# Performance work log

Hardware: AMD Instinct MI355X
Metric: run time of the kernel (lower is better)

Reference implementation:

```python
import jax, jax.numpy as jnp
import numpy as np

D_MODEL, N_HEADS, D_FF = 1024, 16, 4096
NUM_FAMILIES, DICT_SIZE = 64, 16384
B, T = 2, 2048
EPS = 1e-6


def setup_inputs() -> dict:
    key = jax.random.key(0)
    ks = jax.random.split(key, 16)
    s = 0.02
    return {
        "x": jax.random.normal(ks[0], (B, T, D_MODEL), jnp.float32),
        "top_k": 8,
        "proto": jax.random.normal(ks[1], (NUM_FAMILIES, D_MODEL), jnp.float32) * s,
        "family_gate_w": jax.random.normal(ks[2], (NUM_FAMILIES, D_MODEL), jnp.float32) * s,
        "dict_w": jax.random.normal(ks[3], (DICT_SIZE, D_MODEL), jnp.float32) * s,
        "enc_w": jax.random.normal(ks[4], (DICT_SIZE, D_MODEL), jnp.float32) * s,
        "wq": jax.random.normal(ks[5], (D_MODEL, D_MODEL), jnp.float32) * s,
        "wk": jax.random.normal(ks[6], (D_MODEL, D_MODEL), jnp.float32) * s,
        "wv": jax.random.normal(ks[7], (D_MODEL, D_MODEL), jnp.float32) * s,
        "wo": jax.random.normal(ks[8], (D_MODEL, D_MODEL), jnp.float32) * s,
        "rel_templates": jax.random.normal(ks[9], (N_HEADS, D_MODEL // N_HEADS, D_MODEL // N_HEADS), jnp.float32) * s,
        "gate_proj_w": jax.random.normal(ks[10], (D_FF, D_MODEL), jnp.float32) * s,
        "up_proj_w": jax.random.normal(ks[11], (D_FF, D_MODEL), jnp.float32) * s,
        "down_proj_w": jax.random.normal(ks[12], (D_MODEL, D_FF), jnp.float32) * s,
        "norm1_w": jnp.ones((D_MODEL,), jnp.float32),
        "norm2_w": jnp.ones((D_MODEL,), jnp.float32),
        "bias_corr": jnp.zeros((D_MODEL,), jnp.float32),
    }


def _hc_norm(x, w):
    rms = jnp.sqrt(jnp.mean(x * x, axis=-1, keepdims=True) + EPS)
    return w * x / rms, jnp.mean(rms)


def _block(x, top_k, proto, family_gate_w, dict_w, enc_w, wq, wk, wv, wo,
           rel_templates, gate_proj_w, up_proj_w, down_proj_w,
           norm1_w, norm2_w, bias_corr):
    b, t, d = x.shape
    h = rel_templates.shape[0]
    dh = d // h
    m = dict_w.shape[0]

    # FamilyBasisPool
    family_scores = jax.nn.softmax(x @ family_gate_w.T, axis=-1)   # [b,t,K]
    basis = jnp.einsum('btk,kd->btd', family_scores, proto)

    # SparseOffsetDict on residual
    resid = x - basis
    coeffs = resid @ enc_w.T                                        # [b,t,M]
    topk_vals, topk_idx = jax.lax.top_k(coeffs, top_k)              # [b,t,k]
    # sparse scatter + einsum == gather rows of dictionary and weight them
    offset = jnp.einsum('btk,btkd->btd', topk_vals, dict_w[topk_idx])
    sparsity = jnp.sum(jnp.abs(topk_vals)) / (b * t * m)

    x_rec = basis + offset + bias_corr
    normed, e1 = _hc_norm(x_rec, norm1_w)

    # RelationProtocolLayer (k modulated by per-head templates)
    q = (normed @ wq.T).reshape(b, t, h, dh).transpose(0, 2, 1, 3)  # [b,h,t,dh]
    k = (normed @ wk.T).reshape(b, t, h, dh).transpose(0, 2, 1, 3)
    v = (normed @ wv.T).reshape(b, t, h, dh).transpose(0, 2, 1, 3)
    k_mod = jnp.einsum('bhtd,hde->bhte', k, rel_templates)
    attn = jax.nn.softmax(jnp.einsum('bhqd,bhkd->bhqk', q, k_mod) / jnp.sqrt(jnp.float32(dh)), axis=-1)
    out = jnp.einsum('bhqk,bhkd->bhqd', attn, v)
    out = out.transpose(0, 2, 1, 3).reshape(b, t, d) @ wo.T
    x = x + out

    normed2, e2 = _hc_norm(x, norm2_w)

    # ContextGatedRouter (sigmoid gate * silu up)
    gate = jax.nn.sigmoid(normed2 @ gate_proj_w.T)
    up = jax.nn.silu(normed2 @ up_proj_w.T)
    routed = (gate * up) @ down_proj_w.T
    x = x + routed
    return x, attn, family_scores, sparsity, e1, e2


def reference(x, top_k, proto, family_gate_w, dict_w, enc_w, wq, wk, wv, wo,
              rel_templates, gate_proj_w, up_proj_w, down_proj_w,
              norm1_w, norm2_w, bias_corr):
    return _block(x, top_k, proto, family_gate_w, dict_w, enc_w, wq, wk, wv, wo,
                  rel_templates, gate_proj_w, up_proj_w, down_proj_w,
                  norm1_w, norm2_w, bias_corr)
```

## Files before the change

kernel.cpp:

```cpp
#include <hip/hip_runtime.h>
#include <float.h>
#include <math.h>

#define D 1024
#define NF 64
#define MDICT 16384
#define NH 16
#define DH 64
#define TT 2048
#define ROWS 4096
#define DFF 4096

#define OUT_X     0LL
#define OUT_ATTN  4194304LL
#define OUT_FS    138412032LL
#define OUT_SPARS 138674176LL
#define OUT_E1    138674177LL
#define OUT_E2    138674178LL

typedef __attribute__((ext_vector_type(8))) short short8;
typedef __attribute__((ext_vector_type(4))) float f32x4;

__device__ inline unsigned short f2bf(float f) {
    unsigned int u = __float_as_uint(f);
    u = u + 0x7FFFu + ((u >> 16) & 1u);
    return (unsigned short)(u >> 16);
}
__device__ inline float bf2f(unsigned int s) {
    return __uint_as_float(s << 16);
}

__device__ inline float blk_sum(float v) {
    __shared__ float sb[4];
    int lane = threadIdx.x & 63, w = threadIdx.x >> 6;
#pragma unroll
    for (int o = 32; o; o >>= 1) v += __shfl_down(v, o);
    if (lane == 0) sb[w] = v;
    __syncthreads();
    float s = sb[0] + sb[1] + sb[2] + sb[3];
    __syncthreads();
    return s;
}

__device__ inline float blk_max(float v) {
    __shared__ float sm[4];
    int lane = threadIdx.x & 63, w = threadIdx.x >> 6;
#pragma unroll
    for (int o = 32; o; o >>= 1) v = fmaxf(v, __shfl_down(v, o));
    if (lane == 0) sm[w] = v;
    __syncthreads();
    float s = fmaxf(fmaxf(sm[0], sm[1]), fmaxf(sm[2], sm[3]));
    __syncthreads();
    return s;
}

template<int BM, int BN, bool OBF, bool ACONV>
__global__ __launch_bounds__(256) void gemm_mfma(
    const void* __restrict__ Abv, const unsigned short* __restrict__ Bb,
    void* __restrict__ Cbv, const float* __restrict__ addCb,
    int K, int lda, int ldb, int ldc, float alpha, int batchH,
    long long aOut, long long aIn, long long bOut, long long bIn,
    long long cOut, long long cIn)
{
    int z = blockIdx.z;
    int zo = z / batchH, zi = z - zo * batchH;
    long long aoff = zo * aOut + zi * aIn;
    const unsigned short* B = Bb + zo * bOut + zi * bIn;
    long long cbase = zo * cOut + zi * cIn;
    const float* addC = addCb ? (addCb + cbase) : nullptr;

    __shared__ __align__(16) unsigned short As[BM * 32];
    __shared__ __align__(16) unsigned short Bs[BN * 32];

    int tid = threadIdx.x;
    int lane = tid & 63, wave = tid >> 6;
    int wr = wave >> 1, wc = wave & 1;
    long long r0 = (long long)blockIdx.y * BM;
    long long c0 = (long long)blockIdx.x * BN;

    constexpr int TI = BM / 32;
    constexpr int TJ = BN / 32;
    constexpr int RA = BM * 4 / 256;
    constexpr int RB = BN * 4 / 256;

    f32x4 acc[TI][TJ] = {};
    int lm = lane & 15;
    int kq = (lane >> 4) * 8;

    for (int k0 = 0; k0 < K; k0 += 32) {
        __syncthreads();
#pragma unroll
        for (int r = 0; r < RB; r++) {
            int q = r * 256 + tid;
            const unsigned short* gp = B + (c0 + (q >> 2)) * (long long)ldb + k0 + (q & 3) * 8;
            unsigned short* lp = Bs + (r * 256 + (tid & 192)) * 8;
            __builtin_amdgcn_global_load_lds(
                (const __attribute__((address_space(1))) void*)gp,
                (__attribute__((address_space(3))) void*)lp, 16, 0, 0);
        }
        if (ACONV) {
            const float* A = (const float*)Abv + aoff;
#pragma unroll
            for (int r = 0; r < RA; r++) {
                int q = r * 256 + tid;
                const float* gp = A + (r0 + (q >> 2)) * (long long)lda + k0 + (q & 3) * 8;
                float4 v0 = *(const float4*)gp;
                float4 v1 = *(const float4*)(gp + 4);
                short8 f;
                f[0] = (short)f2bf(v0.x); f[1] = (short)f2bf(v0.y);
                f[2] = (short)f2bf(v0.z); f[3] = (short)f2bf(v0.w);
                f[4] = (short)f2bf(v1.x); f[5] = (short)f2bf(v1.y);
                f[6] = (short)f2bf(v1.z); f[7] = (short)f2bf(v1.w);
                *(short8*)&As[q * 8] = f;
            }
        } else {
            const unsigned short* A = (const unsigned short*)Abv + aoff;
#pragma unroll
            for (int r = 0; r < RA; r++) {
                int q = r * 256 + tid;
                const unsigned short* gp = A + (r0 + (q >> 2)) * (long long)lda + k0 + (q & 3) * 8;
                unsigned short* lp = As + (r * 256 + (tid & 192)) * 8;
                __builtin_amdgcn_global_load_lds(
                    (const __attribute__((address_space(1))) void*)gp,
                    (__attribute__((address_space(3))) void*)lp, 16, 0, 0);
            }
        }
        __syncthreads();
        short8 af[TI], bfr[TJ];
#pragma unroll
        for (int i = 0; i < TI; i++)
            af[i] = *(const short8*)&As[(wr * (BM / 2) + i * 16 + lm) * 32 + kq];
#pragma unroll
        for (int j = 0; j < TJ; j++)
            bfr[j] = *(const short8*)&Bs[(wc * (BN / 2) + j * 16 + lm) * 32 + kq];
#pragma unroll
        for (int i = 0; i < TI; i++)
#pragma unroll
            for (int j = 0; j < TJ; j++)
                acc[i][j] = __builtin_amdgcn_mfma_f32_16x16x32_bf16(af[i], bfr[j], acc[i][j], 0, 0, 0);
    }

#pragma unroll
    for (int i = 0; i < TI; i++) {
#pragma unroll
        for (int r = 0; r < 4; r++) {
            long long row = r0 + wr * (BM / 2) + i * 16 + (lane >> 4) * 4 + r;
#pragma unroll
            for (int j = 0; j < TJ; j++) {
                long long col = c0 + wc * (BN / 2) + j * 16 + lm;
                long long idx = row * (long long)ldc + col;
                float v = alpha * acc[i][j][r];
                if (addC) v += addC[idx];
                if (OBF) ((unsigned short*)Cbv)[cbase + idx] = f2bf(v);
                else     ((float*)Cbv)[cbase + idx] = v;
            }
        }
    }
}

__global__ __launch_bounds__(256) void cvt_bf16_kernel(
    const float* __restrict__ in, unsigned short* __restrict__ out, long long n4)
{
    long long i = (long long)blockIdx.x * 256 + threadIdx.x;
    long long stride = (long long)gridDim.x * 256;
    for (; i < n4; i += stride) {
        float4 v = ((const float4*)in)[i];
        uint2 p;
        p.x = (unsigned)f2bf(v.x) | ((unsigned)f2bf(v.y) << 16);
        p.y = (unsigned)f2bf(v.z) | ((unsigned)f2bf(v.w) << 16);
        ((uint2*)out)[i] = p;
    }
}

__global__ __launch_bounds__(64) void family_kernel(
    const float* __restrict__ x, const float* __restrict__ fgw,
    float* __restrict__ fs_out)
{
    __shared__ float xs[D];
    int r = blockIdx.x, f = threadIdx.x;
    const float4* x4 = (const float4*)(x + (long long)r * D);
    float4* xs4 = (float4*)xs;
#pragma unroll
    for (int i = 0; i < 4; i++) xs4[f + 64 * i] = x4[f + 64 * i];
    __syncthreads();
    const float4* w4 = (const float4*)(fgw + (long long)f * D);
    float acc = 0.f;
#pragma unroll 8
    for (int d = 0; d < D / 4; d++) {
        float4 w = w4[d];
        float4 xv = xs4[d];
        acc += w.x * xv.x + w.y * xv.y + w.z * xv.z + w.w * xv.w;
    }
    float mx = acc;
#pragma unroll
    for (int o = 32; o; o >>= 1) mx = fmaxf(mx, __shfl_xor(mx, o));
    float e = __expf(acc - mx);
    float s = e;
#pragma unroll
    for (int o = 32; o; o >>= 1) s += __shfl_xor(s, o);
    fs_out[(long long)r * NF + f] = e / s;
}

__global__ __launch_bounds__(256) void basis_kernel(
    const float* __restrict__ x, const float* __restrict__ fs,
    const float* __restrict__ proto, float* __restrict__ basis,
    unsigned short* __restrict__ resid_bf)
{
    __shared__ float Ss[NF];
    int r = blockIdx.x, tid = threadIdx.x;
    if (tid < NF) Ss[tid] = fs[(long long)r * NF + tid];
    __syncthreads();
    float4 acc = {0.f, 0.f, 0.f, 0.f};
    const float4* p4 = (const float4*)proto;
#pragma unroll 8
    for (int k = 0; k < NF; k++) {
        float s = Ss[k];
        float4 p = p4[k * (D / 4) + tid];
        acc.x += s * p.x; acc.y += s * p.y; acc.z += s * p.z; acc.w += s * p.w;
    }
    long long base = (long long)r * (D / 4) + tid;
    float4 xv = ((const float4*)x)[base];
    ((float4*)basis)[base] = acc;
    uint2 rp;
    rp.x = (unsigned)f2bf(xv.x - acc.x) | ((unsigned)f2bf(xv.y - acc.y) << 16);
    rp.y = (unsigned)f2bf(xv.z - acc.z) | ((unsigned)f2bf(xv.w - acc.w) << 16);
    ((uint2*)resid_bf)[base] = rp;
}

__device__ inline void ins8(float v, int idx, float* vs, int* is) {
    if (v <= vs[7]) return;
    vs[7] = v; is[7] = idx;
#pragma unroll
    for (int j = 7; j > 0; j--) {
        if (vs[j] > vs[j - 1]) {
            float tv = vs[j]; vs[j] = vs[j - 1]; vs[j - 1] = tv;
            int ti = is[j]; is[j] = is[j - 1]; is[j - 1] = ti;
        }
    }
}

__global__ __launch_bounds__(256) void topk_kernel(
    const float* __restrict__ coeffs, float* __restrict__ tkv,
    int* __restrict__ tki, float* __restrict__ spars_acc)
{
    __shared__ float sv[2624];
    __shared__ int   si[2624];
    int r = blockIdx.x, tid = threadIdx.x;
    const float* row = coeffs + (long long)r * MDICT;
    float vs[8]; int is[8];
#pragma unroll
    for (int j = 0; j < 8; j++) { vs[j] = -FLT_MAX; is[j] = -1; }
    for (int s = 0; s < MDICT / 256; s++) {
        int col = s * 256 + tid;
        ins8(row[col], col, vs, is);
    }
#pragma unroll
    for (int j = 0; j < 8; j++) { sv[tid * 8 + j] = vs[j]; si[tid * 8 + j] = is[j]; }
    __syncthreads();
    if (tid < 64) {
#pragma unroll
        for (int j = 0; j < 8; j++) { vs[j] = -FLT_MAX; is[j] = -1; }
        for (int e = tid * 32; e < tid * 32 + 32; e++) ins8(sv[e], si[e], vs, is);
#pragma unroll
        for (int j = 0; j < 8; j++) { sv[2048 + tid * 8 + j] = vs[j]; si[2048 + tid * 8 + j] = is[j]; }
    }
    __syncthreads();
    if (tid < 8) {
#pragma unroll
        for (int j = 0; j < 8; j++) { vs[j] = -FLT_MAX; is[j] = -1; }
        for (int e = 2048 + tid * 64; e < 2048 + tid * 64 + 64; e++) ins8(sv[e], si[e], vs, is);
#pragma unroll
        for (int j = 0; j < 8; j++) { sv[2560 + tid * 8 + j] = vs[j]; si[2560 + tid * 8 + j] = is[j]; }
    }
    __syncthreads();
    if (tid == 0) {
#pragma unroll
        for (int j = 0; j < 8; j++) { vs[j] = -FLT_MAX; is[j] = -1; }
        for (int e = 2560; e < 2624; e++) ins8(sv[e], si[e], vs, is);
        float s = 0.f;
#pragma unroll
        for (int j = 0; j < 8; j++) {
            tkv[r * 8 + j] = vs[j];
            tki[r * 8 + j] = is[j];
            s += fabsf(vs[j]);
        }
        atomicAdd(spars_acc, s);
    }
}

__global__ __launch_bounds__(256) void xrec_norm_kernel(
    const float* __restrict__ basis, const float* __restrict__ dictw,
    const float* __restrict__ bias, const float* __restrict__ nw,
    const float* __restrict__ tkv, const int* __restrict__ tki,
    unsigned short* __restrict__ normed_bf, float* __restrict__ e_acc)
{
    int r = blockIdx.x, tid = threadIdx.x;
    float vals[8]; int idxs[8];
#pragma unroll
    for (int j = 0; j < 8; j++) { vals[j] = tkv[r * 8 + j]; idxs[j] = tki[r * 8 + j]; }
    long long base = (long long)r * (D / 4) + tid;
    float4 acc = ((const float4*)basis)[base];
    float4 bv = ((const float4*)bias)[tid];
    acc.x += bv.x; acc.y += bv.y; acc.z += bv.z; acc.w += bv.w;
#pragma unroll
    for (int j = 0; j < 8; j++) {
        float4 dv = ((const float4*)dictw)[(long long)idxs[j] * (D / 4) + tid];
        float v = vals[j];
        acc.x += v * dv.x; acc.y += v * dv.y; acc.z += v * dv.z; acc.w += v * dv.w;
    }
    float ss = acc.x * acc.x + acc.y * acc.y + acc.z * acc.z + acc.w * acc.w;
    float tot = blk_sum(ss);
    float rms = sqrtf(tot / (float)D + 1e-6f);
    if (tid == 0) atomicAdd(e_acc, rms);
    float inv = 1.f / rms;
    float4 wv = ((const float4*)nw)[tid];
    uint2 o;
    o.x = (unsigned)f2bf(acc.x * wv.x * inv) | ((unsigned)f2bf(acc.y * wv.y * inv) << 16);
    o.y = (unsigned)f2bf(acc.z * wv.z * inv) | ((unsigned)f2bf(acc.w * wv.w * inv) << 16);
    ((uint2*)normed_bf)[base] = o;
}

__global__ __launch_bounds__(256) void rmsnorm_kernel(
    const float* __restrict__ xin, const float* __restrict__ nw,
    unsigned short* __restrict__ xout_bf, float* __restrict__ e_acc)
{
    int r = blockIdx.x, tid = threadIdx.x;
    long long base = (long long)r * (D / 4) + tid;
    float4 v = ((const float4*)xin)[base];
    float ss = v.x * v.x + v.y * v.y + v.z * v.z + v.w * v.w;
    float tot = blk_sum(ss);
    float rms = sqrtf(tot / (float)D + 1e-6f);
    if (tid == 0) atomicAdd(e_acc, rms);
    float inv = 1.f / rms;
    float4 wv = ((const float4*)nw)[tid];
    uint2 o;
    o.x = (unsigned)f2bf(v.x * wv.x * inv) | ((unsigned)f2bf(v.y * wv.y * inv) << 16);
    o.y = (unsigned)f2bf(v.z * wv.z * inv) | ((unsigned)f2bf(v.w * wv.w * inv) << 16);
    ((uint2*)xout_bf)[base] = o;
}

__global__ __launch_bounds__(256) void kmod_kernel(
    const unsigned short* __restrict__ kb, const float* __restrict__ rel,
    unsigned short* __restrict__ kmod_bf)
{
    __shared__ float Rs[64 * 64];
    int z = blockIdx.y;
    int b = z >> 4, h = z & 15;
    int tid = threadIdx.x;
    const float4* r4 = (const float4*)(rel + (long long)h * 4096);
    float4* Rs4 = (float4*)Rs;
#pragma unroll
    for (int i = 0; i < 4; i++) Rs4[tid + 256 * i] = r4[tid + 256 * i];
    __syncthreads();
    int e = tid & 63, tl = tid >> 6;
    int t = blockIdx.x * 4 + tl;
    const unsigned short* krow = kb + ((long long)(b * TT + t)) * D + h * DH;
    float acc = 0.f;
#pragma unroll
    for (int d4 = 0; d4 < 16; d4++) {
        uint2 p = *(const uint2*)&krow[d4 * 4];
        acc += bf2f(p.x & 0xFFFFu) * Rs[(d4 * 4 + 0) * 64 + e];
        acc += bf2f(p.x >> 16)     * Rs[(d4 * 4 + 1) * 64 + e];
        acc += bf2f(p.y & 0xFFFFu) * Rs[(d4 * 4 + 2) * 64 + e];
        acc += bf2f(p.y >> 16)     * Rs[(d4 * 4 + 3) * 64 + e];
    }
    kmod_bf[(long long)z * (TT * DH) + t * 64 + e] = f2bf(acc);
}

__global__ __launch_bounds__(256) void vtrans_kernel(
    const unsigned short* __restrict__ vb, unsigned short* __restrict__ vT)
{
    __shared__ unsigned short tile[64][68];
    int z = blockIdx.y, b = z >> 4, h = z & 15;
    int t0 = blockIdx.x * 64;
    int tid = threadIdx.x;
    int tr = tid >> 4;
    int dc = (tid & 15) * 4;
#pragma unroll
    for (int r = 0; r < 4; r++) {
        int t = tr + r * 16;
        uint2 p = *(const uint2*)&vb[((long long)(b * TT + t0 + t)) * D + h * DH + dc];
        tile[t][dc] = (unsigned short)(p.x & 0xFFFFu);
        tile[t][dc + 1] = (unsigned short)(p.x >> 16);
        tile[t][dc + 2] = (unsigned short)(p.y & 0xFFFFu);
        tile[t][dc + 3] = (unsigned short)(p.y >> 16);
    }
    __syncthreads();
#pragma unroll
    for (int r = 0; r < 4; r++) {
        int d = tr + r * 16;
        int t = (tid & 15) * 4;
        uint2 p;
        p.x = (unsigned)tile[t][d] | ((unsigned)tile[t + 1][d] << 16);
        p.y = (unsigned)tile[t + 2][d] | ((unsigned)tile[t + 3][d] << 16);
        *(uint2*)&vT[(long long)z * 64 * TT + (long long)d * TT + t0 + t] = p;
    }
}

__global__ __launch_bounds__(256) void softmax_kernel(float* __restrict__ attn)
{
    long long row = blockIdx.x;
    float4* p4 = (float4*)(attn + row * TT);
    int tid = threadIdx.x;
    float4 v0 = p4[tid], v1 = p4[tid + 256];
    float mx = fmaxf(fmaxf(fmaxf(v0.x, v0.y), fmaxf(v0.z, v0.w)),
                     fmaxf(fmaxf(v1.x, v1.y), fmaxf(v1.z, v1.w)));
    mx = blk_max(mx);
    v0.x = __expf(v0.x - mx); v0.y = __expf(v0.y - mx);
    v0.z = __expf(v0.z - mx); v0.w = __expf(v0.w - mx);
    v1.x = __expf(v1.x - mx); v1.y = __expf(v1.y - mx);
    v1.z = __expf(v1.z - mx); v1.w = __expf(v1.w - mx);
    float s = v0.x + v0.y + v0.z + v0.w + v1.x + v1.y + v1.z + v1.w;
    s = blk_sum(s);
    float inv = 1.f / s;
    v0.x *= inv; v0.y *= inv; v0.z *= inv; v0.w *= inv;
    v1.x *= inv; v1.y *= inv; v1.z *= inv; v1.w *= inv;
    p4[tid] = v0; p4[tid + 256] = v1;
}

__global__ __launch_bounds__(256) void gateup_kernel(
    unsigned short* __restrict__ g, const unsigned short* __restrict__ u, long long n4)
{
    long long i = (long long)blockIdx.x * 256 + threadIdx.x;
    long long stride = (long long)gridDim.x * 256;
    for (; i < n4; i += stride) {
        uint2 gp = ((uint2*)g)[i];
        uint2 up = ((const uint2*)u)[i];
        float gv[4] = { bf2f(gp.x & 0xFFFFu), bf2f(gp.x >> 16), bf2f(gp.y & 0xFFFFu), bf2f(gp.y >> 16) };
        float uv[4] = { bf2f(up.x & 0xFFFFu), bf2f(up.x >> 16), bf2f(up.y & 0xFFFFu), bf2f(up.y >> 16) };
        unsigned short h[4];
#pragma unroll
        for (int j = 0; j < 4; j++) {
            float r = (1.f / (1.f + __expf(-gv[j]))) * uv[j] * (1.f / (1.f + __expf(-uv[j])));
            h[j] = f2bf(r);
        }
        uint2 o;
        o.x = (unsigned)h[0] | ((unsigned)h[1] << 16);
        o.y = (unsigned)h[2] | ((unsigned)h[3] << 16);
        ((uint2*)g)[i] = o;
    }
}

__global__ void finalize_kernel(const float* __restrict__ scal, float* __restrict__ out)
{
    out[OUT_SPARS] = scal[0] / (float)((double)ROWS * (double)MDICT);
    out[OUT_E1] = scal[1] / (float)ROWS;
    out[OUT_E2] = scal[2] / (float)ROWS;
}

extern "C" void kernel_launch(void* const* d_in, const int* in_sizes, int n_in,
                              void* d_out, int out_size, void* d_ws, size_t ws_size,
                              hipStream_t stream) {
    const float* x     = (const float*)d_in[0];
    const float* proto = (const float*)d_in[2];
    const float* fgw   = (const float*)d_in[3];
    const float* dictw = (const float*)d_in[4];
    const float* encw  = (const float*)d_in[5];
    const float* wq    = (const float*)d_in[6];
    const float* wk    = (const float*)d_in[7];
    const float* wv    = (const float*)d_in[8];
    const float* wo    = (const float*)d_in[9];
    const float* rel   = (const float*)d_in[10];
    const float* gatew = (const float*)d_in[11];
    const float* upw   = (const float*)d_in[12];
    const float* downw = (const float*)d_in[13];
    const float* n1w   = (const float*)d_in[14];
    const float* n2w   = (const float*)d_in[15];
    const float* bias  = (const float*)d_in[16];
    float* out = (float*)d_out;
    float* ws  = (float*)d_ws;

    float*          basisf  = ws + 0;
    unsigned short* kb_bf   = (unsigned short*)(ws + 4194304);
    unsigned short* resid_bf= (unsigned short*)(ws + 6291456);
    unsigned short* norm_bf = (unsigned short*)(ws + 8388608);
    unsigned short* qb_bf   = (unsigned short*)(ws + 10485760);
    unsigned short* vb_bf   = (unsigned short*)(ws + 12582912);
    unsigned short* kmod_bf = (unsigned short*)(ws + 14680064);
    unsigned short* vT_bf   = (unsigned short*)(ws + 16777216);
    unsigned short* encw_bf = (unsigned short*)(ws + 18874368);
    unsigned short* up_bf   = (unsigned short*)(ws + 27262976);
    unsigned short* wq_bf   = (unsigned short*)(ws + 35651584);
    unsigned short* wk_bf   = (unsigned short*)(ws + 36175872);
    unsigned short* wv_bf   = (unsigned short*)(ws + 36700160);
    unsigned short* wo_bf   = (unsigned short*)(ws + 37224448);
    unsigned short* gatew_bf= (unsigned short*)(ws + 37748736);
    unsigned short* upw_bf  = (unsigned short*)(ws + 39845888);
    unsigned short* downw_bf= (unsigned short*)(ws + 41943040);
    float*          tkv     = ws + 44040192;
    int*            tki     = (int*)(ws + 44072960);
    float*          scal    = ws + 44105728;
    unsigned short* ctx_bf  = resid_bf;
    unsigned short* gate_bf = encw_bf;
    float*          xmid    = basisf;

    float* fs   = out + OUT_FS;
    float* attn = out + OUT_ATTN;
    float* coeffs = attn;

    hipMemsetAsync(scal, 0, 3 * sizeof(float), stream);

    cvt_bf16_kernel<<<2048, 256, 0, stream>>>(encw, encw_bf, (long long)MDICT * D / 4);
    cvt_bf16_kernel<<<256, 256, 0, stream>>>(wq, wq_bf, (long long)D * D / 4);
    cvt_bf16_kernel<<<256, 256, 0, stream>>>(wk, wk_bf, (long long)D * D / 4);
    cvt_bf16_kernel<<<256, 256, 0, stream>>>(wv, wv_bf, (long long)D * D / 4);
    cvt_bf16_kernel<<<256, 256, 0, stream>>>(wo, wo_bf, (long long)D * D / 4);
    cvt_bf16_kernel<<<1024, 256, 0, stream>>>(gatew, gatew_bf, (long long)DFF * D / 4);
    cvt_bf16_kernel<<<1024, 256, 0, stream>>>(upw, upw_bf, (long long)DFF * D / 4);
    cvt_bf16_kernel<<<1024, 256, 0, stream>>>(downw, downw_bf, (long long)D * DFF / 4);

    family_kernel<<<ROWS, 64, 0, stream>>>(x, fgw, fs);
    basis_kernel<<<ROWS, 256, 0, stream>>>(x, fs, proto, basisf, resid_bf);
    gemm_mfma<128, 128, false, false><<<dim3(128, 32, 1), 256, 0, stream>>>(
        resid_bf, encw_bf, coeffs, nullptr, D, D, D, MDICT, 1.f, 1, 0, 0, 0, 0, 0, 0);
    topk_kernel<<<ROWS, 256, 0, stream>>>(coeffs, tkv, tki, scal + 0);
    xrec_norm_kernel<<<ROWS, 256, 0, stream>>>(basisf, dictw, bias, n1w, tkv, tki, norm_bf, scal + 1);
    gemm_mfma<128, 128, true, false><<<dim3(8, 32, 1), 256, 0, stream>>>(
        norm_bf, wq_bf, qb_bf, nullptr, D, D, D, D, 1.f, 1, 0, 0, 0, 0, 0, 0);
    gemm_mfma<128, 128, true, false><<<dim3(8, 32, 1), 256, 0, stream>>>(
        norm_bf, wk_bf, kb_bf, nullptr, D, D, D, D, 1.f, 1, 0, 0, 0, 0, 0, 0);
    gemm_mfma<128, 128, true, false><<<dim3(8, 32, 1), 256, 0, stream>>>(
        norm_bf, wv_bf, vb_bf, nullptr, D, D, D, D, 1.f, 1, 0, 0, 0, 0, 0, 0);
    kmod_kernel<<<dim3(TT / 4, 32), 256, 0, stream>>>(kb_bf, rel, kmod_bf);
    vtrans_kernel<<<dim3(TT / 64, 32), 256, 0, stream>>>(vb_bf, vT_bf);
    gemm_mfma<128, 128, false, false><<<dim3(16, 16, 32), 256, 0, stream>>>(
        qb_bf, kmod_bf, attn, nullptr, DH, D, DH, TT, 0.125f, NH,
        (long long)TT * D, 64LL,
        (long long)NH * TT * DH, (long long)TT * DH,
        (long long)NH * TT * TT, (long long)TT * TT);
    softmax_kernel<<<32 * TT, 256, 0, stream>>>(attn);
    gemm_mfma<128, 64, true, true><<<dim3(1, 16, 32), 256, 0, stream>>>(
        attn, vT_bf, ctx_bf, nullptr, TT, TT, TT, D, 1.f, NH,
        (long long)NH * TT * TT, (long long)TT * TT,
        (long long)NH * DH * TT, (long long)DH * TT,
        (long long)TT * D, 64LL);
    gemm_mfma<128, 128, false, false><<<dim3(8, 32, 1), 256, 0, stream>>>(
        ctx_bf, wo_bf, xmid, x, D, D, D, D, 1.f, 1, 0, 0, 0, 0, 0, 0);
    rmsnorm_kernel<<<ROWS, 256, 0, stream>>>(xmid, n2w, norm_bf, scal + 2);
    gemm_mfma<128, 128, true, false><<<dim3(32, 32, 1), 256, 0, stream>>>(
        norm_bf, gatew_bf, gate_bf, nullptr, D, D, D, DFF, 1.f, 1, 0, 0, 0, 0, 0, 0);
    gemm_mfma<128, 128, true, false><<<dim3(32, 32, 1), 256, 0, stream>>>(
        norm_bf, upw_bf, up_bf, nullptr, D, D, D, DFF, 1.f, 1, 0, 0, 0, 0, 0, 0);
    gateup_kernel<<<4096, 256, 0, stream>>>(gate_bf, up_bf, (long long)ROWS * DFF / 4);
    gemm_mfma<128, 128, false, false><<<dim3(8, 32, 1), 256, 0, stream>>>(
        gate_bf, downw_bf, out + OUT_X, xmid, DFF, DFF, DFF, D, 1.f, 1, 0, 0, 0, 0, 0, 0);
    finalize_kernel<<<1, 1, 0, stream>>>(scal, out);
}
```

Baseline: 2.287 ms.

## Fuse QK^T, softmax and PV into one two-pass attention kernel

```diff
diff --git a/kernel.cpp b/kernel.cpp
--- a/kernel.cpp
+++ b/kernel.cpp
@@ -38,18 +38,6 @@
     if (lane == 0) sb[w] = v;
     __syncthreads();
     float s = sb[0] + sb[1] + sb[2] + sb[3];
-    __syncthreads();
-    return s;
-}
-
-__device__ inline float blk_max(float v) {
-    __shared__ float sm[4];
-    int lane = threadIdx.x & 63, w = threadIdx.x >> 6;
-#pragma unroll
-    for (int o = 32; o; o >>= 1) v = fmaxf(v, __shfl_down(v, o));
-    if (lane == 0) sm[w] = v;
-    __syncthreads();
-    float s = fmaxf(fmaxf(sm[0], sm[1]), fmaxf(sm[2], sm[3]));
     __syncthreads();
     return s;
 }
@@ -397,25 +385,207 @@
     }
 }
 
-__global__ __launch_bounds__(256) void softmax_kernel(float* __restrict__ attn)
-{
-    long long row = blockIdx.x;
-    float4* p4 = (float4*)(attn + row * TT);
-    int tid = threadIdx.x;
-    float4 v0 = p4[tid], v1 = p4[tid + 256];
-    float mx = fmaxf(fmaxf(fmaxf(v0.x, v0.y), fmaxf(v0.z, v0.w)),
-                     fmaxf(fmaxf(v1.x, v1.y), fmaxf(v1.z, v1.w)));
-    mx = blk_max(mx);
-    v0.x = __expf(v0.x - mx); v0.y = __expf(v0.y - mx);
-    v0.z = __expf(v0.z - mx); v0.w = __expf(v0.w - mx);
-    v1.x = __expf(v1.x - mx); v1.y = __expf(v1.y - mx);
-    v1.z = __expf(v1.z - mx); v1.w = __expf(v1.w - mx);
-    float s = v0.x + v0.y + v0.z + v0.w + v1.x + v1.y + v1.z + v1.w;
-    s = blk_sum(s);
-    float inv = 1.f / s;
-    v0.x *= inv; v0.y *= inv; v0.z *= inv; v0.w *= inv;
-    v1.x *= inv; v1.y *= inv; v1.z *= inv; v1.w *= inv;
-    p4[tid] = v0; p4[tid + 256] = v1;
+__global__ __launch_bounds__(256, 2) void attn_fused_kernel(
+    const unsigned short* __restrict__ qb,
+    const unsigned short* __restrict__ kmod,
+    const unsigned short* __restrict__ vT,
+    float* __restrict__ attn,
+    unsigned short* __restrict__ ctx)
+{
+    constexpr int QS_LD = 72;
+    constexpr int PS_LD = 136;
+    __shared__ __align__(16) unsigned short Qs[128 * QS_LD];
+    __shared__ __align__(16) unsigned short Ks[128 * QS_LD];
+    __shared__ __align__(16) unsigned short Ps[128 * PS_LD];
+    __shared__ float sm_h[2][128];
+    __shared__ float sl_h[2][128];
+
+    const int z = blockIdx.y;
+    const int b = z >> 4, h = z & 15;
+    const int q0 = blockIdx.x * 128;
+    const int tid = threadIdx.x;
+    const int lane = tid & 63;
+    const int wave = tid >> 6;
+    const int wr = wave >> 1, wc = wave & 1;
+    const int lm = lane & 15, q4 = lane >> 4;
+    const int kq = q4 * 8;
+
+    {
+        const unsigned short* qbase = qb + ((long long)(b * TT + q0)) * D + h * DH;
+#pragma unroll
+        for (int rr = 0; rr < 4; rr++) {
+            int q = rr * 256 + tid;
+            int row = q >> 3, seg = q & 7;
+            short8 v = *(const short8*)(qbase + (long long)row * D + seg * 8);
+            *(short8*)&Qs[row * QS_LD + seg * 8] = v;
+        }
+    }
+
+    const unsigned short* kz = kmod + (long long)z * (TT * DH);
+
+    float m_loc[4][4], l_loc[4][4];
+#pragma unroll
+    for (int i = 0; i < 4; i++)
+#pragma unroll
+        for (int r = 0; r < 4; r++) { m_loc[i][r] = -FLT_MAX; l_loc[i][r] = 0.f; }
+
+    for (int kt = 0; kt < 16; kt++) {
+        __syncthreads();
+#pragma unroll
+        for (int rr = 0; rr < 4; rr++) {
+            int q = rr * 256 + tid;
+            int row = q >> 3, seg = q & 7;
+            short8 v = *(const short8*)(kz + (long long)(kt * 128 + row) * DH + seg * 8);
+            *(short8*)&Ks[row * QS_LD + seg * 8] = v;
+        }
+        __syncthreads();
+        f32x4 acc[4][4] = {};
+#pragma unroll
+        for (int ks = 0; ks < 2; ks++) {
+            short8 af[4], bfk[4];
+#pragma unroll
+            for (int i = 0; i < 4; i++)
+                af[i] = *(const short8*)&Qs[(wr * 64 + i * 16 + lm) * QS_LD + ks * 32 + kq];
+#pragma unroll
+            for (int j = 0; j < 4; j++)
+                bfk[j] = *(const short8*)&Ks[(wc * 64 + j * 16 + lm) * QS_LD + ks * 32 + kq];
+#pragma unroll
+            for (int i = 0; i < 4; i++)
+#pragma unroll
+                for (int j = 0; j < 4; j++)
+                    acc[i][j] = __builtin_amdgcn_mfma_f32_16x16x32_bf16(af[i], bfk[j], acc[i][j], 0, 0, 0);
+        }
+#pragma unroll
+        for (int i = 0; i < 4; i++)
+#pragma unroll
+            for (int r = 0; r < 4; r++) {
+                float v0 = acc[i][0][r] * 0.125f;
+                float v1 = acc[i][1][r] * 0.125f;
+                float v2 = acc[i][2][r] * 0.125f;
+                float v3 = acc[i][3][r] * 0.125f;
+                float tmax = fmaxf(fmaxf(v0, v1), fmaxf(v2, v3));
+                float mo = m_loc[i][r];
+                float mn = fmaxf(mo, tmax);
+                l_loc[i][r] = l_loc[i][r] * __expf(mo - mn)
+                            + __expf(v0 - mn) + __expf(v1 - mn)
+                            + __expf(v2 - mn) + __expf(v3 - mn);
+                m_loc[i][r] = mn;
+            }
+    }
+
+#pragma unroll
+    for (int off = 1; off <= 8; off <<= 1) {
+#pragma unroll
+        for (int i = 0; i < 4; i++)
+#pragma unroll
+            for (int r = 0; r < 4; r++) {
+                float mo = __shfl_xor(m_loc[i][r], off);
+                float lo = __shfl_xor(l_loc[i][r], off);
+                float mn = fmaxf(m_loc[i][r], mo);
+                l_loc[i][r] = l_loc[i][r] * __expf(m_loc[i][r] - mn) + lo * __expf(mo - mn);
+                m_loc[i][r] = mn;
+            }
+    }
+    if (lm == 0) {
+#pragma unroll
+        for (int i = 0; i < 4; i++)
+#pragma unroll
+            for (int r = 0; r < 4; r++) {
+                int row = wr * 64 + i * 16 + q4 * 4 + r;
+                sm_h[wc][row] = m_loc[i][r];
+                sl_h[wc][row] = l_loc[i][r];
+            }
+    }
+    __syncthreads();
+    float Mf[4][4], Linv[4][4];
+#pragma unroll
+    for (int i = 0; i < 4; i++)
+#pragma unroll
+        for (int r = 0; r < 4; r++) {
+            int row = wr * 64 + i * 16 + q4 * 4 + r;
+            float m0 = sm_h[0][row], m1 = sm_h[1][row];
+            float l0 = sl_h[0][row], l1 = sl_h[1][row];
+            float mn = fmaxf(m0, m1);
+            float L = l0 * __expf(m0 - mn) + l1 * __expf(m1 - mn);
+            Mf[i][r] = mn;
+            Linv[i][r] = 1.f / L;
+        }
+
+    const unsigned short* vz = vT + (long long)z * (64 * TT);
+    float* az = attn + (long long)z * ((long long)TT * TT);
+    f32x4 acc_o[4][2] = {};
+
+    for (int kt = 0; kt < 16; kt++) {
+        __syncthreads();
+#pragma unroll
+        for (int rr = 0; rr < 4; rr++) {
+            int q = rr * 256 + tid;
+            int row = q >> 3, seg = q & 7;
+            short8 v = *(const short8*)(kz + (long long)(kt * 128 + row) * DH + seg * 8);
+            *(short8*)&Ks[row * QS_LD + seg * 8] = v;
+        }
+        short8 bv[2][4];
+#pragma unroll
+        for (int j = 0; j < 2; j++)
+#pragma unroll
+            for (int ks = 0; ks < 4; ks++)
+                bv[j][ks] = *(const short8*)(vz + (long long)(wc * 32 + j * 16 + lm) * TT
+                                             + kt * 128 + ks * 32 + kq);
+        __syncthreads();
+        f32x4 acc[4][4] = {};
+#pragma unroll
+        for (int ks = 0; ks < 2; ks++) {
+            short8 af[4], bfk[4];
+#pragma unroll
+            for (int i = 0; i < 4; i++)
+                af[i] = *(const short8*)&Qs[(wr * 64 + i * 16 + lm) * QS_LD + ks * 32 + kq];
+#pragma unroll
+            for (int j = 0; j < 4; j++)
+                bfk[j] = *(const short8*)&Ks[(wc * 64 + j * 16 + lm) * QS_LD + ks * 32 + kq];
+#pragma unroll
+            for (int i = 0; i < 4; i++)
+#pragma unroll
+                for (int j = 0; j < 4; j++)
+                    acc[i][j] = __builtin_amdgcn_mfma_f32_16x16x32_bf16(af[i], bfk[j], acc[i][j], 0, 0, 0);
+        }
+#pragma unroll
+        for (int i = 0; i < 4; i++)
+#pragma unroll
+            for (int r = 0; r < 4; r++) {
+                int row = wr * 64 + i * 16 + q4 * 4 + r;
+                float* arow = az + (long long)(q0 + row) * TT + kt * 128 + wc * 64 + lm;
+#pragma unroll
+                for (int j = 0; j < 4; j++) {
+                    float p = __expf(acc[i][j][r] * 0.125f - Mf[i][r]) * Linv[i][r];
+                    arow[j * 16] = p;
+                    Ps[row * PS_LD + wc * 64 + j * 16 + lm] = f2bf(p);
+                }
+            }
+        __syncthreads();
+#pragma unroll
+        for (int ks = 0; ks < 4; ks++) {
+            short8 paf[4];
+#pragma unroll
+            for (int i = 0; i < 4; i++)
+                paf[i] = *(const short8*)&Ps[(wr * 64 + i * 16 + lm) * PS_LD + ks * 32 + kq];
+#pragma unroll
+            for (int i = 0; i < 4; i++)
+#pragma unroll
+                for (int j = 0; j < 2; j++)
+                    acc_o[i][j] = __builtin_amdgcn_mfma_f32_16x16x32_bf16(paf[i], bv[j][ks], acc_o[i][j], 0, 0, 0);
+        }
+    }
+
+#pragma unroll
+    for (int i = 0; i < 4; i++)
+#pragma unroll
+        for (int r = 0; r < 4; r++) {
+            int row = wr * 64 + i * 16 + q4 * 4 + r;
+            long long crow = ((long long)(b * TT + q0 + row)) * D + h * DH;
+#pragma unroll
+            for (int j = 0; j < 2; j++)
+                ctx[crow + wc * 32 + j * 16 + lm] = f2bf(acc_o[i][j][r]);
+        }
 }
 
 __global__ __launch_bounds__(256) void gateup_kernel(
@@ -428,15 +598,15 @@
         uint2 up = ((const uint2*)u)[i];
         float gv[4] = { bf2f(gp.x & 0xFFFFu), bf2f(gp.x >> 16), bf2f(gp.y & 0xFFFFu), bf2f(gp.y >> 16) };
         float uv[4] = { bf2f(up.x & 0xFFFFu), bf2f(up.x >> 16), bf2f(up.y & 0xFFFFu), bf2f(up.y >> 16) };
-        unsigned short h[4];
+        unsigned short hh[4];
 #pragma unroll
         for (int j = 0; j < 4; j++) {
             float r = (1.f / (1.f + __expf(-gv[j]))) * uv[j] * (1.f / (1.f + __expf(-uv[j])));
-            h[j] = f2bf(r);
+            hh[j] = f2bf(r);
         }
         uint2 o;
-        o.x = (unsigned)h[0] | ((unsigned)h[1] << 16);
-        o.y = (unsigned)h[2] | ((unsigned)h[3] << 16);
+        o.x = (unsigned)hh[0] | ((unsigned)hh[1] << 16);
+        o.y = (unsigned)hh[2] | ((unsigned)hh[3] << 16);
         ((uint2*)g)[i] = o;
     }
 }
@@ -523,17 +693,8 @@
         norm_bf, wv_bf, vb_bf, nullptr, D, D, D, D, 1.f, 1, 0, 0, 0, 0, 0, 0);
     kmod_kernel<<<dim3(TT / 4, 32), 256, 0, stream>>>(kb_bf, rel, kmod_bf);
     vtrans_kernel<<<dim3(TT / 64, 32), 256, 0, stream>>>(vb_bf, vT_bf);
-    gemm_mfma<128, 128, false, false><<<dim3(16, 16, 32), 256, 0, stream>>>(
-        qb_bf, kmod_bf, attn, nullptr, DH, D, DH, TT, 0.125f, NH,
-        (long long)TT * D, 64LL,
-        (long long)NH * TT * DH, (long long)TT * DH,
-        (long long)NH * TT * TT, (long long)TT * TT);
-    softmax_kernel<<<32 * TT, 256, 0, stream>>>(attn);
-    gemm_mfma<128, 64, true, true><<<dim3(1, 16, 32), 256, 0, stream>>>(
-        attn, vT_bf, ctx_bf, nullptr, TT, TT, TT, D, 1.f, NH,
-        (long long)NH * TT * TT, (long long)TT * TT,
-        (long long)NH * DH * TT, (long long)DH * TT,
-        (long long)TT * D, 64LL);
+    attn_fused_kernel<<<dim3(TT / 128, 32), 256, 0, stream>>>(
+        qb_bf, kmod_bf, vT_bf, attn, ctx_bf);
     gemm_mfma<128, 128, false, false><<<dim3(8, 32, 1), 256, 0, stream>>>(
         ctx_bf, wo_bf, xmid, x, D, D, D, D, 1.f, 1, 0, 0, 0, 0, 0, 0);
     rmsnorm_kernel<<<ROWS, 256, 0, stream>>>(xmid, n2w, norm_bf, scal + 2);
```

Result: faster. 2.026 ms (-11.4%).
